# Performance work log

Measured on AMD Instinct MI355X. Metric: run time of the kernel, lower is better.

## Reference

```python
import jax, jax.numpy as jnp
import numpy as np

GROUP_MANTISSA = 8
GROUP_SIZE = 36


def bfp_quantize(x, mantissa=GROUP_MANTISSA, group_size=GROUP_SIZE):
    """Block floating point: flatten, group consecutive group_size elements,
    share the max exponent within each group, keep `mantissa` mantissa bits."""
    flat = x.reshape(-1)
    n = flat.shape[0]
    pad = (-n) % group_size
    f = jnp.pad(flat, (0, pad)).reshape(-1, group_size)  # [G, group_size]
    m = jnp.max(jnp.abs(f), axis=1, keepdims=True)       # group max magnitude
    safe_m = jnp.where(m > 0, m, jnp.ones_like(m))
    e = jnp.floor(jnp.log2(safe_m))                      # shared exponent
    scale = jnp.exp2(e - (mantissa - 1))                 # LSB step for the group
    q = jnp.round(f / scale) * scale
    q = jnp.where(m > 0, q, jnp.zeros_like(q))
    return q.reshape(-1)[:n].reshape(x.shape)


def setup_inputs() -> dict:
    key = jax.random.key(0)
    kx, kw, kb = jax.random.split(key, 3)
    x = jax.random.normal(kx, (32, 64, 112, 112), dtype=jnp.float32)
    # kaiming-uniform-ish scale for a 3x3x64 fan-in
    fan_in = 64 * 3 * 3
    bound = 1.0 / np.sqrt(fan_in)
    weight = jax.random.uniform(kw, (64, 64, 3, 3), dtype=jnp.float32, minval=-bound, maxval=bound) * np.sqrt(3.0)
    bias = jax.random.uniform(kb, (64,), dtype=jnp.float32, minval=-bound, maxval=bound)
    return {"x": x, "weight": weight, "bias": bias}


def reference(x, weight, bias):
    xq = bfp_quantize(x)
    wq = bfp_quantize(weight)
    out = jax.lax.conv_general_dilated(
        xq, wq,
        window_strides=(1, 1),
        padding=((1, 1), (1, 1)),
        lhs_dilation=(1, 1),
        rhs_dilation=(1, 1),
        dimension_numbers=("NCHW", "OIHW", "NCHW"),
        feature_group_count=1,
    )
    return out + bias[None, :, None, None]
```

## Files before the change

### kernel.cpp

```cpp
#include <hip/hip_runtime.h>

typedef __attribute__((ext_vector_type(4))) float f32x4;
typedef __attribute__((ext_vector_type(8))) short s16x8;
typedef __attribute__((ext_vector_type(4))) unsigned int u32x4;

#define HW 112
#define ROWS8 (116*8)
#define PLANE8 (112*ROWS8)
#define CHW (64*112*112)
#define X_ELEMS 25690112

#define WT_OFF    53219328
#define ZP_OFF    59001984

__device__ __forceinline__ unsigned short f32_to_bf16_exact(float q) {
    return (unsigned short)(__float_as_uint(q) >> 16);
}
__device__ __forceinline__ unsigned int pack_bf16x2(float a, float b) {
    return __builtin_amdgcn_perm(__float_as_uint(b), __float_as_uint(a), 0x07060302u);
}
__device__ __forceinline__ void scale_from_max(float m, float& scale, float& inv) {
    if (m > 0.f) {
        int e = (int)((__float_as_uint(m) >> 23) & 0xFF) - 127;
        scale = __builtin_ldexpf(1.0f, e - 7);
        inv   = __builtin_ldexpf(1.0f, 7 - e);
    } else { scale = 0.f; inv = 0.f; }
}

__global__ __launch_bounds__(256) void qx_fused(const float* __restrict__ x,
                                                const float* __restrict__ w,
                                                unsigned short* __restrict__ xq8,
                                                unsigned short* __restrict__ wt,
                                                u32x4* __restrict__ zp) {
    __shared__ float vals[8 * 448];
    __shared__ float lmax[1024];
    __shared__ float2 ssc[8][16];
    __shared__ int sgs[8];
    const int tid = threadIdx.x;
    const int b = blockIdx.x;

    if (b >= 7168) {
        if (b == 7168 && tid < 64) zp[tid] = (u32x4){0u, 0u, 0u, 0u};
        int g = (b - 7168) * 256 + tid;
        const float4* p = (const float4*)w + g * 9;
        float vv[36]; float m = 0.f;
        #pragma unroll
        for (int i = 0; i < 9; ++i) {
            float4 v = p[i];
            vv[i*4+0]=v.x; vv[i*4+1]=v.y; vv[i*4+2]=v.z; vv[i*4+3]=v.w;
            m = fmaxf(m, fmaxf(fmaxf(fabsf(v.x), fabsf(v.y)), fmaxf(fabsf(v.z), fabsf(v.w))));
        }
        float s, inv; scale_from_max(m, s, inv);
        #pragma unroll
        for (int j = 0; j < 36; ++j) {
            int flat = g * 36 + j;
            int k = flat / 576, rem = flat % 576;
            int c = rem / 9, pp = rem % 9;
            float q = rintf(vv[j] * inv) * s;
            wt[pp * 4096 + k * 64 + c] = f32_to_bf16_exact(q);
        }
        return;
    }

    const int plane = b / 28, chunk = b - plane * 28;
    const int p0 = chunk * 448;
    const int base_plane = plane * 8 * 12544;

    #pragma unroll
    for (int it = 0; it < 4; ++it) {
        int g = it * 256 + tid;
        int j = g >> 7, gi = g & 127;
        int flat = base_plane + j * 12544 + p0 - 32 + gi * 4;
        float4 v = {0.f, 0.f, 0.f, 0.f};
        if (flat >= 0 && flat < X_ELEMS) v = *(const float4*)(x + flat);
        lmax[g] = fmaxf(fmaxf(fabsf(v.x), fabsf(v.y)), fmaxf(fabsf(v.z), fabsf(v.w)));
        if (gi >= 8 && gi < 120)
            *(f32x4*)&vals[j * 448 + (gi - 8) * 4] = (f32x4){v.x, v.y, v.z, v.w};
    }
    __syncthreads();

    if (tid < 128) {
        int j = tid >> 4, k = tid & 15;
        unsigned a0 = (unsigned)(base_plane + j * 12544 + p0);
        int gstart = (int)(a0 / 36u);
        int gend   = (int)((a0 + 447u) / 36u);
        if (k == 0) sgs[j] = gstart;
        if (gstart + k <= gend) {
            int ps = 36 * (gstart + k) - (int)a0;
            int gb = ps / 4 + 8;
            float m = 0.f;
            #pragma unroll
            for (int q = 0; q < 9; ++q) m = fmaxf(m, lmax[j * 128 + gb + q]);
            float s, inv; scale_from_max(m, s, inv);
            ssc[j][k] = make_float2(s, inv);
        }
    }
    __syncthreads();

    const int hrow0 = chunk * 4;
    #pragma unroll
    for (int it = 0; it < 2; ++it) {
        int s = it * 256 + tid;
        if (s < 464) {
            int h = s / 116, w2 = s - h * 116;
            unsigned short* dst = xq8 + (plane * 112 + hrow0 + h) * ROWS8 + w2 * 8;
            u32x4 o = {0u, 0u, 0u, 0u};
            if (w2 >= 2 && w2 < 114) {
                int dp = h * 112 + (w2 - 2);
                unsigned pbase = (unsigned)(base_plane + p0 + dp);
                float qv[8];
                #pragma unroll
                for (int j = 0; j < 8; ++j) {
                    float v = vals[j * 448 + dp];
                    unsigned g = (pbase + (unsigned)j * 12544u) / 36u;
                    float2 sv = ssc[j][(int)g - sgs[j]];
                    qv[j] = rintf(v * sv.y) * sv.x;
                }
                o.x = pack_bf16x2(qv[0], qv[1]);
                o.y = pack_bf16x2(qv[2], qv[3]);
                o.z = pack_bf16x2(qv[4], qv[5]);
                o.w = pack_bf16x2(qv[6], qv[7]);
            }
            *(u32x4*)dst = o;
        }
    }
}

__global__ __launch_bounds__(256) void conv_mfma(const unsigned short* __restrict__ xq8,
                                                 const unsigned short* __restrict__ wt,
                                                 const float* __restrict__ bias,
                                                 float* __restrict__ out,
                                                 const unsigned short* __restrict__ zp) {
    __shared__ unsigned short xs[2][3328 * 8];
    const int tid = threadIdx.x;
    const int wave = tid >> 6, lane = tid & 63;
    const int wl = lane & 15, quad = lane >> 4;
    const int kg = wave & 1, mg = wave >> 1;
    const int bs = blockIdx.x;

    unsigned pk13[13];
    #pragma unroll
    for (int k = 0; k < 13; ++k) {
        int g = (wave * 13 + k) * 64 + lane;
        if (g < 3200) {
            int oct = g / 400, rem = g - oct * 400;
            int r = rem / 40, pix = rem - r * 40;
            int pixs = pix ^ oct;
            pk13[k] = ((unsigned)r << 24) | (unsigned)(oct * PLANE8 + pixs * 8);
        } else pk13[k] = 0xFF000000u;
    }

    float bv[2];
    #pragma unroll
    for (int j = 0; j < 2; ++j) bv[j] = bias[kg * 32 + j * 16 + wl];
    int pixb[7];
    #pragma unroll
    for (int mti = 0; mti < 7; ++mti) {
        int m = (mg * 7 + mti) * 16 + wl;
        pixb[mti] = (m / 28) * 40 + (m % 28) + 1;
    }

    auto issue = [&](int ti, int bi) {
        int t = bs + 256 * ti;
        int st = ((t & 7) * 224) + (t >> 3);
        int n = st / 56, rem = st - n * 56;
        int h0 = (rem >> 2) * 8, w0 = (rem & 3) * 28;
        const unsigned short* base = xq8 + n * 8 * PLANE8 + w0 * 8;
        #pragma unroll
        for (int k = 0; k < 13; ++k) {
            unsigned pk = pk13[k];
            int r = (int)(pk >> 24);
            int hh = h0 - 1 + r;
            bool ok = (r <= 9) && (hh >= 0) && (hh < HW);
            const unsigned short* src = ok ? (base + (pk & 0xFFFFFFu) + hh * ROWS8) : zp;
            unsigned short* dst = (unsigned short*)&xs[bi][(wave * 13 + k) * 512];
            __builtin_amdgcn_global_load_lds(
                (const __attribute__((address_space(1))) void*)src,
                (__attribute__((address_space(3))) void*)dst, 16, 0, 0);
        }
    };

    issue(0, 0);

    #pragma unroll 1
    for (int i = 0; i < 7; ++i) {
        if (i == 0) asm volatile("s_waitcnt vmcnt(0)" ::: "memory");
        else        asm volatile("s_waitcnt vmcnt(14)" ::: "memory");
        __builtin_amdgcn_s_barrier();
        if (i < 6) issue(i + 1, (i + 1) & 1);

        int t = bs + 256 * i;
        int st = ((t & 7) * 224) + (t >> 3);
        int n = st / 56, rem = st - n * 56;
        int h0 = (rem >> 2) * 8, w0 = (rem & 3) * 28;
        const unsigned short* xb = &xs[i & 1][0];

        f32x4 acc[7][2];
        f32x4 zero = {0.f, 0.f, 0.f, 0.f};
        #pragma unroll
        for (int mti = 0; mti < 7; ++mti) { acc[mti][0] = zero; acc[mti][1] = zero; }

        #pragma unroll
        for (int p = 0; p < 9; ++p) {
            const int dpix = (p / 3) * 40 + (p % 3);
            #pragma unroll
            for (int cs = 0; cs < 2; ++cs) {
                const int oq = cs * 4 + quad;
                s16x8 B0 = *(const s16x8*)(wt + p * 4096 + ((kg * 2 + 0) * 16 + wl) * 64 + cs * 32 + quad * 8);
                s16x8 B1 = *(const s16x8*)(wt + p * 4096 + ((kg * 2 + 1) * 16 + wl) * 64 + cs * 32 + quad * 8);
                s16x8 A[7];
                #pragma unroll
                for (int mti = 0; mti < 7; ++mti) {
                    int pix = pixb[mti] + dpix;
                    A[mti] = *(const s16x8*)(xb + (oq * 400 + (pix ^ oq)) * 8);
                }
                #pragma unroll
                for (int mti = 0; mti < 7; ++mti) {
                    acc[mti][0] = __builtin_amdgcn_mfma_f32_16x16x32_bf16(A[mti], B0, acc[mti][0], 0, 0, 0);
                    acc[mti][1] = __builtin_amdgcn_mfma_f32_16x16x32_bf16(A[mti], B1, acc[mti][1], 0, 0, 0);
                }
            }
        }

        int obase = n * CHW + h0 * HW + w0;
        #pragma unroll
        for (int mti = 0; mti < 7; ++mti) {
            int m0 = (mg * 7 + mti) * 16 + quad * 4;
            int eofs = (m0 / 28) * HW + (m0 % 28);
            #pragma unroll
            for (int j = 0; j < 2; ++j) {
                f32x4 v = acc[mti][j];
                v.x += bv[j]; v.y += bv[j]; v.z += bv[j]; v.w += bv[j];
                *(f32x4*)(out + obase + (kg * 32 + j * 16 + wl) * 12544 + eofs) = v;
            }
        }
    }
}

extern "C" void kernel_launch(void* const* d_in, const int* in_sizes, int n_in,
                              void* d_out, int out_size, void* d_ws, size_t ws_size,
                              hipStream_t stream) {
    const float* x    = (const float*)d_in[0];
    const float* w    = (const float*)d_in[1];
    const float* bias = (const float*)d_in[2];
    float* out = (float*)d_out;
    char* ws = (char*)d_ws;
    unsigned short* xq8 = (unsigned short*)ws;
    unsigned short* wt  = (unsigned short*)(ws + WT_OFF);
    unsigned short* zp  = (unsigned short*)(ws + ZP_OFF);

    hipLaunchKernelGGL(qx_fused,  dim3(7172), dim3(256), 0, stream, x, w, xq8, wt, (u32x4*)zp);
    hipLaunchKernelGGL(conv_mfma, dim3(256),  dim3(256), 0, stream, xq8, wt, bias, out, zp);
}
```

Baseline: 250.0 us.

## Double conv block to 512 threads, splitting M tiles 4/4/3/3 across waves

The conv kernel moves from 4 to 8 waves per block. Each wave group now handles 3–4 M tiles instead of 7, which cuts accumulator registers per wave and adds latency hiding. The LDS fill is spread over 8 waves with 7 chunks each instead of 13. The pipelined partial wait (vmcnt(14)) becomes a full vmcnt(0) wait each iteration, which may reduce overlap of the next tile's load with compute. The 4/4/3/3 split leaves the waves unevenly loaded.

```diff
diff --git a/kernel.cpp b/kernel.cpp
--- a/kernel.cpp
+++ b/kernel.cpp
@@ -126,7 +126,7 @@
     }
 }
 
-__global__ __launch_bounds__(256) void conv_mfma(const unsigned short* __restrict__ xq8,
+__global__ __launch_bounds__(512) void conv_mfma(const unsigned short* __restrict__ xq8,
                                                  const unsigned short* __restrict__ wt,
                                                  const float* __restrict__ bias,
                                                  float* __restrict__ out,
@@ -136,27 +136,30 @@
     const int wave = tid >> 6, lane = tid & 63;
     const int wl = lane & 15, quad = lane >> 4;
     const int kg = wave & 1, mg = wave >> 1;
+    const int mbase = (mg < 2) ? mg * 4 : 8 + (mg - 2) * 3;
+    const int mcnt  = (mg < 2) ? 4 : 3;
     const int bs = blockIdx.x;
 
-    unsigned pk13[13];
-    #pragma unroll
-    for (int k = 0; k < 13; ++k) {
-        int g = (wave * 13 + k) * 64 + lane;
-        if (g < 3200) {
+    unsigned pk7[7];
+    #pragma unroll
+    for (int k = 0; k < 7; ++k) {
+        int cg = wave * 7 + k;
+        int g = cg * 64 + lane;
+        if (cg < 52 && g < 3200) {
             int oct = g / 400, rem = g - oct * 400;
             int r = rem / 40, pix = rem - r * 40;
             int pixs = pix ^ oct;
-            pk13[k] = ((unsigned)r << 24) | (unsigned)(oct * PLANE8 + pixs * 8);
-        } else pk13[k] = 0xFF000000u;
+            pk7[k] = ((unsigned)r << 24) | (unsigned)(oct * PLANE8 + pixs * 8);
+        } else pk7[k] = 0xFF000000u;
     }
 
     float bv[2];
     #pragma unroll
     for (int j = 0; j < 2; ++j) bv[j] = bias[kg * 32 + j * 16 + wl];
-    int pixb[7];
-    #pragma unroll
-    for (int mti = 0; mti < 7; ++mti) {
-        int m = (mg * 7 + mti) * 16 + wl;
+    int pixb[4];
+    #pragma unroll
+    for (int mti = 0; mti < 4; ++mti) {
+        int m = (mbase + mti) * 16 + wl;
         pixb[mti] = (m / 28) * 40 + (m % 28) + 1;
     }
 
@@ -167,16 +170,19 @@
         int h0 = (rem >> 2) * 8, w0 = (rem & 3) * 28;
         const unsigned short* base = xq8 + n * 8 * PLANE8 + w0 * 8;
         #pragma unroll
-        for (int k = 0; k < 13; ++k) {
-            unsigned pk = pk13[k];
-            int r = (int)(pk >> 24);
-            int hh = h0 - 1 + r;
-            bool ok = (r <= 9) && (hh >= 0) && (hh < HW);
-            const unsigned short* src = ok ? (base + (pk & 0xFFFFFFu) + hh * ROWS8) : zp;
-            unsigned short* dst = (unsigned short*)&xs[bi][(wave * 13 + k) * 512];
-            __builtin_amdgcn_global_load_lds(
-                (const __attribute__((address_space(1))) void*)src,
-                (__attribute__((address_space(3))) void*)dst, 16, 0, 0);
+        for (int k = 0; k < 7; ++k) {
+            int cg = wave * 7 + k;
+            if (cg < 52) {
+                unsigned pk = pk7[k];
+                int r = (int)(pk >> 24);
+                int hh = h0 - 1 + r;
+                bool ok = (r <= 9) && (hh >= 0) && (hh < HW);
+                const unsigned short* src = ok ? (base + (pk & 0xFFFFFFu) + hh * ROWS8) : zp;
+                unsigned short* dst = (unsigned short*)&xs[bi][cg * 512];
+                __builtin_amdgcn_global_load_lds(
+                    (const __attribute__((address_space(1))) void*)src,
+                    (__attribute__((address_space(3))) void*)dst, 16, 0, 0);
+            }
         }
     };
 
@@ -184,8 +190,7 @@
 
     #pragma unroll 1
     for (int i = 0; i < 7; ++i) {
-        if (i == 0) asm volatile("s_waitcnt vmcnt(0)" ::: "memory");
-        else        asm volatile("s_waitcnt vmcnt(14)" ::: "memory");
+        asm volatile("s_waitcnt vmcnt(0)" ::: "memory");
         __builtin_amdgcn_s_barrier();
         if (i < 6) issue(i + 1, (i + 1) & 1);
 
@@ -195,10 +200,10 @@
         int h0 = (rem >> 2) * 8, w0 = (rem & 3) * 28;
         const unsigned short* xb = &xs[i & 1][0];
 
-        f32x4 acc[7][2];
+        f32x4 acc[4][2];
         f32x4 zero = {0.f, 0.f, 0.f, 0.f};
         #pragma unroll
-        for (int mti = 0; mti < 7; ++mti) { acc[mti][0] = zero; acc[mti][1] = zero; }
+        for (int mti = 0; mti < 4; ++mti) { acc[mti][0] = zero; acc[mti][1] = zero; }
 
         #pragma unroll
         for (int p = 0; p < 9; ++p) {
@@ -208,32 +213,35 @@
                 const int oq = cs * 4 + quad;
                 s16x8 B0 = *(const s16x8*)(wt + p * 4096 + ((kg * 2 + 0) * 16 + wl) * 64 + cs * 32 + quad * 8);
                 s16x8 B1 = *(const s16x8*)(wt + p * 4096 + ((kg * 2 + 1) * 16 + wl) * 64 + cs * 32 + quad * 8);
-                s16x8 A[7];
-                #pragma unroll
-                for (int mti = 0; mti < 7; ++mti) {
-                    int pix = pixb[mti] + dpix;
-                    A[mti] = *(const s16x8*)(xb + (oq * 400 + (pix ^ oq)) * 8);
+                s16x8 A[4];
+                #pragma unroll
+                for (int mti = 0; mti < 4; ++mti)
+                    if (mti < mcnt) {
+                        int pix = pixb[mti] + dpix;
+                        A[mti] = *(const s16x8*)(xb + (oq * 400 + (pix ^ oq)) * 8);
+                    }
+                #pragma unroll
+                for (int mti = 0; mti < 4; ++mti)
+                    if (mti < mcnt) {
+                        acc[mti][0] = __builtin_amdgcn_mfma_f32_16x16x32_bf16(A[mti], B0, acc[mti][0], 0, 0, 0);
+                        acc[mti][1] = __builtin_amdgcn_mfma_f32_16x16x32_bf16(A[mti], B1, acc[mti][1], 0, 0, 0);
+                    }
+            }
+        }
+
+        int obase = n * CHW + h0 * HW + w0;
+        #pragma unroll
+        for (int mti = 0; mti < 4; ++mti)
+            if (mti < mcnt) {
+                int m0 = (mbase + mti) * 16 + quad * 4;
+                int eofs = (m0 / 28) * HW + (m0 % 28);
+                #pragma unroll
+                for (int j = 0; j < 2; ++j) {
+                    f32x4 v = acc[mti][j];
+                    v.x += bv[j]; v.y += bv[j]; v.z += bv[j]; v.w += bv[j];
+                    *(f32x4*)(out + obase + (kg * 32 + j * 16 + wl) * 12544 + eofs) = v;
                 }
-                #pragma unroll
-                for (int mti = 0; mti < 7; ++mti) {
-                    acc[mti][0] = __builtin_amdgcn_mfma_f32_16x16x32_bf16(A[mti], B0, acc[mti][0], 0, 0, 0);
-                    acc[mti][1] = __builtin_amdgcn_mfma_f32_16x16x32_bf16(A[mti], B1, acc[mti][1], 0, 0, 0);
-                }
-            }
-        }
-
-        int obase = n * CHW + h0 * HW + w0;
-        #pragma unroll
-        for (int mti = 0; mti < 7; ++mti) {
-            int m0 = (mg * 7 + mti) * 16 + quad * 4;
-            int eofs = (m0 / 28) * HW + (m0 % 28);
-            #pragma unroll
-            for (int j = 0; j < 2; ++j) {
-                f32x4 v = acc[mti][j];
-                v.x += bv[j]; v.y += bv[j]; v.z += bv[j]; v.w += bv[j];
-                *(f32x4*)(out + obase + (kg * 32 + j * 16 + wl) * 12544 + eofs) = v;
-            }
-        }
+            }
     }
 }
 
@@ -250,5 +258,5 @@
     unsigned short* zp  = (unsigned short*)(ws + ZP_OFF);
 
     hipLaunchKernelGGL(qx_fused,  dim3(7172), dim3(256), 0, stream, x, w, xq8, wt, (u32x4*)zp);
-    hipLaunchKernelGGL(conv_mfma, dim3(256),  dim3(256), 0, stream, xq8, wt, bias, out, zp);
-}
+    hipLaunchKernelGGL(conv_mfma, dim3(256),  dim3(512), 0, stream, xq8, wt, bias, out, zp);
+}
```

New measurement: 271.5 us. 8.6% more time.
